# Kernel tuning notes

Hardware: AMD Instinct MI355X
Metric: run time of the kernel (lower is better)

The kernel has to match this reference:

```python
import jax, jax.numpy as jnp
import numpy as np
from jax import lax

T_STEPS = 16
TAU = 2.0
ALPHA = 4.0  # sigmoid surrogate sharpness
BN_EPS = 1e-5


def conv1d(x, w, b, stride, pad):
    # x: [N,C,L], w: [O,I,K]
    y = lax.conv_general_dilated(x, w, (stride,), [(pad, pad)],
                                 dimension_numbers=('NCH', 'OIH', 'NCH'))
    return y + b[None, :, None]


def maxpool1d(x):  # kernel 3, stride 2, pad 1 (pad value -inf via init)
    return lax.reduce_window(x, -jnp.inf, lax.max, (1, 1, 3), (1, 1, 2),
                             [(0, 0), (0, 0), (1, 1)])


def spike(x):  # heaviside forward (surrogate only matters for bwd)
    return (x >= 0).astype(x.dtype)


def lif(x_seq):
    # multi-step LIF: v += (x - v)/tau (v_reset=0), spike at v>=1, hard reset, detach_reset
    def step(v, x):
        v = v + (x - v) / TAU
        s = spike(v - 1.0)
        v = v * (1.0 - lax.stop_gradient(s))
        return v, s
    _, s_seq = lax.scan(step, jnp.zeros_like(x_seq[0]), x_seq)
    return s_seq


def seq_apply(f, xs):
    # apply stateless layer over [T,B,...] by folding T into batch
    T, B = xs.shape[0], xs.shape[1]
    y = f(xs.reshape((T * B,) + xs.shape[2:]))
    return y.reshape((T, B) + y.shape[1:])


def setup_inputs() -> dict:
    key = jax.random.key(0)
    ks = jax.random.split(key, 12)
    B, L = 256, 4097
    inp = {
        'x': jax.random.normal(ks[0], (B, L), jnp.float32),
        'conv0_w': jax.random.normal(ks[1], (16, 1, 7), jnp.float32) * 0.2,
        'conv0_b': jax.random.normal(ks[2], (16,), jnp.float32) * 0.1,
        'bn_g': jnp.ones((16,), jnp.float32),
        'bn_b': jnp.zeros((16,), jnp.float32),
        'bn_m': jax.random.normal(ks[3], (16,), jnp.float32) * 0.1,
        'bn_v': jnp.ones((16,), jnp.float32),
        'conv1_w': jax.random.normal(ks[4], (32, 16, 5), jnp.float32) * 0.1,
        'conv1_b': jax.random.normal(ks[5], (32,), jnp.float32) * 0.1,
        'conv2_w': jax.random.normal(ks[6], (64, 32, 3), jnp.float32) * 0.1,
        'conv2_b': jax.random.normal(ks[7], (64,), jnp.float32) * 0.1,
        'fc1_w': jax.random.normal(ks[8], (32, 64), jnp.float32) * 0.12,
        'fc1_b': jax.random.normal(ks[9], (32,), jnp.float32) * 0.1,
        'fc2_w': jax.random.normal(ks[10], (5, 32), jnp.float32) * 0.17,
        'fc2_b': jax.random.normal(ks[11], (5,), jnp.float32) * 0.1,
    }
    return inp


def reference(x, conv0_w, conv0_b, bn_g, bn_b, bn_m, bn_v,
              conv1_w, conv1_b, conv2_w, conv2_b,
              fc1_w, fc1_b, fc2_w, fc2_b):
    # ---- static encoder ----
    h = x[:, None, :]                                  # [B,1,4097]
    h = conv1d(h, conv0_w, conv0_b, 2, 3)              # [B,16,2049]
    h = (h - bn_m[None, :, None]) * lax.rsqrt(bn_v + BN_EPS)[None, :, None] \
        * bn_g[None, :, None] + bn_b[None, :, None]
    h = jax.nn.relu(h)
    h = maxpool1d(h)                                   # [B,16,1025]
    # ---- repeat over T timesteps ----
    hs = jnp.broadcast_to(h[None], (T_STEPS,) + h.shape)  # [T,B,16,1025]
    # ---- spiking trunk ----
    hs = seq_apply(lambda a: conv1d(a, conv1_w, conv1_b, 2, 2), hs)  # [T,B,32,513]
    hs = lif(hs)
    hs = seq_apply(maxpool1d, hs)                      # [T,B,32,257]
    hs = seq_apply(lambda a: conv1d(a, conv2_w, conv2_b, 2, 1), hs)  # [T,B,64,129]
    hs = lif(hs)
    # dropout: identity (inference); adaptive avg pool to 1 + flatten
    hs = hs.mean(axis=-1)                              # [T,B,64]
    # ---- classifier ----
    hs = jnp.einsum('tbd,od->tbo', hs, fc1_w) + fc1_b  # [T,B,32]
    hs = lif(hs)
    hs = jnp.einsum('tbd,od->tbo', hs, fc2_w) + fc2_b  # [T,B,5]
    return hs.mean(axis=0)                             # [B,5]
```

## Files before the change

### kernel.cpp

```cpp
#include <hip/hip_runtime.h>
#include <math.h>


#define NB 256
#define LX 4097
#define LQ 2049
#define LP 1025
#define LJ1 513
#define LP1 257
#define LJ2 129

#define M1S 520
#define S2R 132
#define HSW 260

typedef float f32x4 __attribute__((ext_vector_type(4)));

__global__ __launch_bounds__(256) void kF_front(const float* __restrict__ x,
                                                const float* __restrict__ w0,
                                                const float* __restrict__ b0,
                                                const float* __restrict__ bng,
                                                const float* __restrict__ bnb,
                                                const float* __restrict__ bnm,
                                                const float* __restrict__ bnv,
                                                const float* __restrict__ w1,
                                                const float* __restrict__ b1,
                                                unsigned short* __restrict__ m1,
                                                const float* __restrict__ w2,
                                                float* __restrict__ w2t) {
  __shared__ __align__(16) float xs[1052];
  __shared__ __align__(16) float hs[16 * HSW];
  __shared__ __align__(16) float wl[2560];
  __shared__ float w0s[112];
  __shared__ float cpar[64];
  __shared__ float rs_l[16];
  int bid = blockIdx.x;
  int b = bid / 5, jt = bid % 5;
  int J0 = jt * 128;
  int Pstart = 2 * J0 - 2;
  int tid = threadIdx.x;

  if (tid < 16) rs_l[tid] = (float)(1.0 / sqrt((double)bnv[tid] + 1e-5));
  {
    const float* xb = x + (size_t)b * LX;
    int xoff = 4 * Pstart - 5;
    for (int i = tid; i < 1052; i += 256) {
      int gi = xoff + i;
      xs[i] = (gi >= 0 && gi < LX) ? xb[gi] : 0.f;
    }
    for (int i = tid; i < 2560; i += 256) {
      int c = i & 31, r = i >> 5;
      wl[i] = w1[c * 80 + r];
    }
    if (tid < 112) w0s[tid] = w0[tid];
    if (tid >= 128 && tid < 192) {
      int i = tid - 128;
      int c = i >> 2, e = i & 3;
      float v = (e == 0) ? bnm[c] : (e == 1) ? bng[c] : (e == 2) ? bnb[c] : b0[c];
      cpar[i] = v;
    }
  }
  __syncthreads();

  for (int item = tid; item < 16 * 261; item += 256) {
    int c = item / 261, dp = item - c * 261;
    int p = Pstart + dp;
    float hm = 0.f;
    if (p >= 0 && p < LP) {
      const f32x4* xv = (const f32x4*)(xs + 4 * dp);
      f32x4 a = xv[0], bq = xv[1], cq = xv[2];
      float win[12] = {a.x, a.y, a.z, a.w, bq.x, bq.y, bq.z, bq.w,
                       cq.x, cq.y, cq.z, cq.w};
      float m = cpar[4 * c], g = cpar[4 * c + 1], bb = cpar[4 * c + 2],
            bc = cpar[4 * c + 3];
      float rs = rs_l[c];
      float wv[7];
#pragma unroll
      for (int k = 0; k < 7; ++k) wv[k] = w0s[c * 7 + k];
      float best = -INFINITY;
#pragma unroll
      for (int dq = -1; dq <= 1; ++dq) {
        int q = 2 * p + dq;
        if (q < 0 || q >= LQ) continue;
        float s = 0.f;
        int base = 2 * dq + 2;
#pragma unroll
        for (int k = 0; k < 7; ++k) s = fmaf(win[base + k], wv[k], s);
        float y = s + bc;
        y = (y - m) * rs * g + bb;
        y = fmaxf(y, 0.f);
        best = fmaxf(best, y);
      }
      hm = best;
    }
    hs[c * HSW + dp] = hm;
  }
  __syncthreads();

  {
    int c = tid & 31, jg = tid >> 5;
    int jbase = J0 + jg * 16;
    if (jbase <= 512) {
      float acc[16];
#pragma unroll
      for (int i = 0; i < 16; ++i) acc[i] = 0.f;

      for (int ic = 0; ic < 16; ++ic) {
        float win[36];
        const f32x4* row = (const f32x4*)(hs + ic * HSW + 32 * jg);
#pragma unroll
        for (int i = 0; i < 9; ++i) {
          f32x4 v = row[i];
          win[4 * i] = v.x; win[4 * i + 1] = v.y;
          win[4 * i + 2] = v.z; win[4 * i + 3] = v.w;
        }
        float wv[5];
#pragma unroll
        for (int k = 0; k < 5; ++k) wv[k] = wl[(ic * 5 + k) * 32 + c];
#pragma unroll
        for (int j = 0; j < 16; ++j) {
#pragma unroll
          for (int k = 0; k < 5; ++k) acc[j] = fmaf(win[2 * j + k], wv[k], acc[j]);
        }
      }

      float bc = b1[c];
      unsigned mskv[16];
#pragma unroll
      for (int j = 0; j < 16; ++j) {
        float xin = acc[j] + bc;
        float v = 0.f; unsigned mm = 0;
#pragma unroll
        for (int t = 0; t < 16; ++t) {
          v = v + (xin - v) * 0.5f;
          if (v >= 1.f) { mm |= (1u << t); v = 0.f; }
        }
        mskv[j] = mm;
      }
      size_t rowo = ((size_t)b * 32 + c) * M1S + jbase;
      if (jbase + 15 < LJ1) {
        uint4 u0, u1;
        u0.x = mskv[0] | (mskv[1] << 16);
        u0.y = mskv[2] | (mskv[3] << 16);
        u0.z = mskv[4] | (mskv[5] << 16);
        u0.w = mskv[6] | (mskv[7] << 16);
        u1.x = mskv[8] | (mskv[9] << 16);
        u1.y = mskv[10] | (mskv[11] << 16);
        u1.z = mskv[12] | (mskv[13] << 16);
        u1.w = mskv[14] | (mskv[15] << 16);
        *(uint4*)(m1 + rowo) = u0;
        *(uint4*)(m1 + rowo + 8) = u1;
      } else {
        for (int j = 0; j < 16; ++j)
          if (jbase + j < LJ1) m1[rowo + j] = (unsigned short)mskv[j];
      }
    }
  }

  if (bid < 16) {
    for (int idx = bid * 256 + tid; idx < 64 * 32 * 3; idx += 4096) {
      int k = idx % 3; int r = idx / 3; int c = r % 32; int oc = r / 32;
      w2t[(c * 3 + k) * 64 + oc] = w2[idx];
    }
  }
}

__global__ __launch_bounds__(256) void kD_conv2_lif(const unsigned short* __restrict__ m1,
                                                    const float* __restrict__ w2t_g,
                                                    const float* __restrict__ b2,
                                                    unsigned short* __restrict__ s2) {
  __shared__ __align__(16) float F[288 * 20];
  __shared__ unsigned mval[288];
  __shared__ unsigned short mbuf[32 * 20];
  int bid = blockIdx.x;
  int b = bid / 33, jt = bid % 33;
  int j0 = jt * 4;
  int tid = threadIdx.x;
  int w = tid >> 6;
  int lane = tid & 63;

  const unsigned short* m1b = m1 + (size_t)b * 32 * M1S;
  int qbase = 4 * j0 - 3;
  for (int i = tid; i < 1024; i += 256) {
    int c = i >> 5, u = i & 31;
    if (u < 20) {
      int q = qbase + u;
      mbuf[c * 20 + u] = (q >= 0 && q <= 512) ? m1b[(size_t)c * M1S + q] : (unsigned short)0;
    }
  }
  __syncthreads();

  for (int it = tid; it < 288; it += 256) {
    int c = it / 9, idx = it - c * 9;
    int p = 2 * j0 - 1 + idx;
    unsigned m = 0;
    if (p >= 0 && p < LP1) {
      const unsigned short* mr = mbuf + c * 20;
      int l0 = 2 * idx;
      m = (unsigned)mr[l0] | (unsigned)mr[l0 + 1] | (unsigned)mr[l0 + 2];
    }
    mval[it] = m;
    f32x4* Fr = (f32x4*)(F + it * 20);
    f32x4 f0, f1, f2, f3;
    f0.x = (float)(m & 1u);         f0.y = (float)((m >> 1) & 1u);
    f0.z = (float)((m >> 2) & 1u);  f0.w = (float)((m >> 3) & 1u);
    f1.x = (float)((m >> 4) & 1u);  f1.y = (float)((m >> 5) & 1u);
    f1.z = (float)((m >> 6) & 1u);  f1.w = (float)((m >> 7) & 1u);
    f2.x = (float)((m >> 8) & 1u);  f2.y = (float)((m >> 9) & 1u);
    f2.z = (float)((m >> 10) & 1u); f2.w = (float)((m >> 11) & 1u);
    f3.x = (float)((m >> 12) & 1u); f3.y = (float)((m >> 13) & 1u);
    f3.z = (float)((m >> 14) & 1u); f3.w = (float)((m >> 15) & 1u);
    Fr[0] = f0; Fr[1] = f1; Fr[2] = f2; Fr[3] = f3;
  }
  __syncthreads();

  unsigned bits;
  {
    bool nz = false;
    if (lane < 32) {
      int base9 = lane * 9 + 2 * w;
      nz = (mval[base9] | mval[base9 + 1] | mval[base9 + 2]) != 0u;
    }
    bits = (unsigned)__ballot(nz);
  }

  float acc[16];
#pragma unroll
  for (int t = 0; t < 16; ++t) acc[t] = 0.f;

  const float* wrow = w2t_g + lane;
  while (bits) {
    int c = __builtin_ctz(bits);
    bits &= bits - 1;
    int base9 = c * 9 + 2 * w;
    unsigned mv0 = mval[base9];
    unsigned mv1 = mval[base9 + 1];
    unsigned mv2 = mval[base9 + 2];
    const float* wr = wrow + c * 192;
    const float* Fb = F + base9 * 20;
    if (mv0) {
      float wv = wr[0];
      const f32x4* Fp = (const f32x4*)Fb;
      f32x4 fv[4];
      fv[0] = Fp[0]; fv[1] = Fp[1]; fv[2] = Fp[2]; fv[3] = Fp[3];
#pragma unroll
      for (int t = 0; t < 16; ++t) acc[t] = fmaf(wv, fv[t >> 2][t & 3], acc[t]);
    }
    if (mv1) {
      float wv = wr[64];
      const f32x4* Fp = (const f32x4*)(Fb + 20);
      f32x4 fv[4];
      fv[0] = Fp[0]; fv[1] = Fp[1]; fv[2] = Fp[2]; fv[3] = Fp[3];
#pragma unroll
      for (int t = 0; t < 16; ++t) acc[t] = fmaf(wv, fv[t >> 2][t & 3], acc[t]);
    }
    if (mv2) {
      float wv = wr[128];
      const f32x4* Fp = (const f32x4*)(Fb + 40);
      f32x4 fv[4];
      fv[0] = Fp[0]; fv[1] = Fp[1]; fv[2] = Fp[2]; fv[3] = Fp[3];
#pragma unroll
      for (int t = 0; t < 16; ++t) acc[t] = fmaf(wv, fv[t >> 2][t & 3], acc[t]);
    }
  }

  int j = j0 + w;
  if (j < LJ2) {
    float bc = b2[lane];
    float v = 0.f; unsigned mm = 0;
#pragma unroll
    for (int t = 0; t < 16; ++t) {
      float xin = acc[t] + bc;
      v = v + (xin - v) * 0.5f;
      if (v >= 1.f) { mm |= (1u << t); v = 0.f; }
    }
    s2[((size_t)b * S2R + j) * 64 + lane] = (unsigned short)mm;
  }
}

__global__ __launch_bounds__(256) void kE_head(const unsigned short* __restrict__ s2,
                                               const float* __restrict__ fc1w,
                                               const float* __restrict__ fc1b,
                                               const float* __restrict__ fc2w,
                                               const float* __restrict__ fc2b,
                                               float* __restrict__ out) {
  __shared__ float meanL[16][64];
  __shared__ unsigned s3m[32];
  int b = blockIdx.x;
  int tid = threadIdx.x;
  int oc = tid >> 2, part = tid & 3;

  int jstart = (part == 0) ? 0 : 33 + (part - 1) * 32;
  int jcount = (part == 0) ? 33 : 32;
  const unsigned short* base = s2 + (size_t)b * S2R * 64 + oc;
  int cnt[16];
#pragma unroll
  for (int t = 0; t < 16; ++t) cnt[t] = 0;
  for (int u = 0; u < jcount; ++u) {
    unsigned m = base[(size_t)(jstart + u) * 64];
#pragma unroll
    for (int t = 0; t < 16; ++t) cnt[t] += (int)((m >> t) & 1u);
  }
#pragma unroll
  for (int t = 0; t < 16; ++t) {
    cnt[t] += __shfl_xor(cnt[t], 1);
    cnt[t] += __shfl_xor(cnt[t], 2);
  }
  if (part == 0) {
#pragma unroll
    for (int t = 0; t < 16; ++t) meanL[t][oc] = (float)cnt[t] / 129.f;
  }
  __syncthreads();

  if (tid < 32) {
    int o = tid;
    const float* wrow = fc1w + o * 64;
    float bb = fc1b[o];
    float v = 0.f;
    unsigned msk = 0;
    for (int t = 0; t < 16; ++t) {
      float s = 0.f;
      for (int d = 0; d < 64; ++d) s = fmaf(meanL[t][d], wrow[d], s);
      float xin = s + bb;
      v = v + (xin - v) * 0.5f;
      if (v >= 1.f) { msk |= (1u << t); v = 0.f; }
    }
    s3m[o] = msk;
  }
  __syncthreads();

  if (tid < 5) {
    int q = tid;
    const float* wrow = fc2w + q * 32;
    float bb = fc2b[q];
    float accs = 0.f;
    for (int t = 0; t < 16; ++t) {
      float s = 0.f;
      for (int o = 0; o < 32; ++o) s += (((s3m[o] >> t) & 1u) ? wrow[o] : 0.f);
      accs += (s + bb);
    }
    out[b * 5 + q] = accs / 16.f;
  }
}

extern "C" void kernel_launch(void* const* d_in, const int* in_sizes, int n_in,
                              void* d_out, int out_size, void* d_ws, size_t ws_size,
                              hipStream_t stream) {
  const float* x   = (const float*)d_in[0];
  const float* w0  = (const float*)d_in[1];
  const float* b0  = (const float*)d_in[2];
  const float* bng = (const float*)d_in[3];
  const float* bnb = (const float*)d_in[4];
  const float* bnm = (const float*)d_in[5];
  const float* bnv = (const float*)d_in[6];
  const float* w1  = (const float*)d_in[7];
  const float* b1  = (const float*)d_in[8];
  const float* w2  = (const float*)d_in[9];
  const float* b2  = (const float*)d_in[10];
  const float* f1w = (const float*)d_in[11];
  const float* f1b = (const float*)d_in[12];
  const float* f2w = (const float*)d_in[13];
  const float* f2b = (const float*)d_in[14];
  float* out = (float*)d_out;

  char* ws = (char*)d_ws;
  size_t sz_m1 = (size_t)NB * 32 * M1S * 2;
  size_t sz_s2 = (size_t)NB * S2R * 64 * 2;
  size_t off_s2 = sz_m1;
  size_t off_w2 = off_s2 + sz_s2;
  if (ws_size < off_w2 + 6144 * 4) return;

  unsigned short* m1 = (unsigned short*)ws;
  unsigned short* s2 = (unsigned short*)(ws + off_s2);
  float* w2t = (float*)(ws + off_w2);

  kF_front<<<NB * 5, 256, 0, stream>>>(x, w0, b0, bng, bnb, bnm, bnv, w1, b1, m1, w2, w2t);
  kD_conv2_lif<<<NB * 33, 256, 0, stream>>>(m1, w2t, b2, s2);
  kE_head<<<NB, 256, 0, stream>>>(s2, f1w, f1b, f2w, f2b, out);
}
```

Baseline: 121.1 us.

## Halve conv2 block size with 2 outputs per thread; restructure front and head reductions

The conv2+LIF kernel now runs 128 threads per block. Each lane computes two output channels for one output position, so each F row loaded from LDS feeds two accumulator sets, and the per-channel zero-skip becomes a coarser whole-row check. The front encoder loop assigns one channel per 16-thread group and hoists per-channel weights and BN parameters out of the item loop. The head now does a coalesced per-warp count with an LDS reduction instead of shuffles. The costs are higher register pressure and fewer skipped FMAs in kD.

```diff
diff --git a/kernel.cpp b/kernel.cpp
--- a/kernel.cpp
+++ b/kernel.cpp
@@ -62,38 +62,43 @@
   }
   __syncthreads();
 
-  for (int item = tid; item < 16 * 261; item += 256) {
-    int c = item / 261, dp = item - c * 261;
-    int p = Pstart + dp;
-    float hm = 0.f;
-    if (p >= 0 && p < LP) {
-      const f32x4* xv = (const f32x4*)(xs + 4 * dp);
-      f32x4 a = xv[0], bq = xv[1], cq = xv[2];
-      float win[12] = {a.x, a.y, a.z, a.w, bq.x, bq.y, bq.z, bq.w,
-                       cq.x, cq.y, cq.z, cq.w};
-      float m = cpar[4 * c], g = cpar[4 * c + 1], bb = cpar[4 * c + 2],
-            bc = cpar[4 * c + 3];
-      float rs = rs_l[c];
-      float wv[7];
-#pragma unroll
-      for (int k = 0; k < 7; ++k) wv[k] = w0s[c * 7 + k];
-      float best = -INFINITY;
-#pragma unroll
-      for (int dq = -1; dq <= 1; ++dq) {
-        int q = 2 * p + dq;
-        if (q < 0 || q >= LQ) continue;
-        float s = 0.f;
-        int base = 2 * dq + 2;
-#pragma unroll
-        for (int k = 0; k < 7; ++k) s = fmaf(win[base + k], wv[k], s);
-        float y = s + bc;
-        y = (y - m) * rs * g + bb;
-        y = fmaxf(y, 0.f);
-        best = fmaxf(best, y);
-      }
-      hm = best;
-    }
-    hs[c * HSW + dp] = hm;
+  {
+    int c2 = tid >> 4, g2 = tid & 15;
+    float m = cpar[4 * c2], g = cpar[4 * c2 + 1], bb = cpar[4 * c2 + 2],
+          bc = cpar[4 * c2 + 3];
+    float rs = rs_l[c2];
+    float wv[7];
+#pragma unroll
+    for (int k = 0; k < 7; ++k) wv[k] = w0s[c2 * 7 + k];
+#pragma unroll
+    for (int i = 0; i < 17; ++i) {
+      int dp = g2 * 17 + i;
+      if (dp >= 261) break;
+      int p = Pstart + dp;
+      float hm = 0.f;
+      if (p >= 0 && p < LP) {
+        const f32x4* xv = (const f32x4*)(xs + 4 * dp);
+        f32x4 a = xv[0], bq = xv[1], cq = xv[2];
+        float win[12] = {a.x, a.y, a.z, a.w, bq.x, bq.y, bq.z, bq.w,
+                         cq.x, cq.y, cq.z, cq.w};
+        float best = -INFINITY;
+#pragma unroll
+        for (int dq = -1; dq <= 1; ++dq) {
+          int q = 2 * p + dq;
+          if (q < 0 || q >= LQ) continue;
+          float s = 0.f;
+          int base = 2 * dq + 2;
+#pragma unroll
+          for (int k = 0; k < 7; ++k) s = fmaf(win[base + k], wv[k], s);
+          float y = s + bc;
+          y = (y - m) * rs * g + bb;
+          y = fmaxf(y, 0.f);
+          best = fmaxf(best, y);
+        }
+        hm = best;
+      }
+      hs[c2 * HSW + dp] = hm;
+    }
   }
   __syncthreads();
 
@@ -165,7 +170,7 @@
   }
 }
 
-__global__ __launch_bounds__(256) void kD_conv2_lif(const unsigned short* __restrict__ m1,
+__global__ __launch_bounds__(128) void kD_conv2_lif(const unsigned short* __restrict__ m1,
                                                     const float* __restrict__ w2t_g,
                                                     const float* __restrict__ b2,
                                                     unsigned short* __restrict__ s2) {
@@ -174,25 +179,27 @@
   __shared__ unsigned short mbuf[32 * 20];
   int bid = blockIdx.x;
   int b = bid / 33, jt = bid % 33;
-  int j0 = jt * 4;
+  int J0 = jt * 4;
   int tid = threadIdx.x;
   int w = tid >> 6;
   int lane = tid & 63;
+  int wh = lane >> 5;
+  int oc0 = lane & 31;
 
   const unsigned short* m1b = m1 + (size_t)b * 32 * M1S;
-  int qbase = 4 * j0 - 3;
-  for (int i = tid; i < 1024; i += 256) {
-    int c = i >> 5, u = i & 31;
-    if (u < 20) {
+  int qbase = 4 * J0 - 3;
+  for (int i = tid; i < 640; i += 128) {
+    int c = i / 20, u = i - c * 20;
+    if (u < 19) {
       int q = qbase + u;
       mbuf[c * 20 + u] = (q >= 0 && q <= 512) ? m1b[(size_t)c * M1S + q] : (unsigned short)0;
     }
   }
   __syncthreads();
 
-  for (int it = tid; it < 288; it += 256) {
+  for (int it = tid; it < 288; it += 128) {
     int c = it / 9, idx = it - c * 9;
-    int p = 2 * j0 - 1 + idx;
+    int p = 2 * J0 - 1 + idx;
     unsigned m = 0;
     if (p >= 0 && p < LP1) {
       const unsigned short* mr = mbuf + c * 20;
@@ -218,63 +225,79 @@
   {
     bool nz = false;
     if (lane < 32) {
-      int base9 = lane * 9 + 2 * w;
-      nz = (mval[base9] | mval[base9 + 1] | mval[base9 + 2]) != 0u;
+      int mb = lane * 9 + 4 * w;
+      unsigned o = mval[mb] | mval[mb + 1] | mval[mb + 2] | mval[mb + 3] | mval[mb + 4];
+      nz = (o != 0u);
     }
     bits = (unsigned)__ballot(nz);
   }
 
-  float acc[16];
-#pragma unroll
-  for (int t = 0; t < 16; ++t) acc[t] = 0.f;
-
-  const float* wrow = w2t_g + lane;
+  float acc0[16], acc1[16];
+#pragma unroll
+  for (int t = 0; t < 16; ++t) { acc0[t] = 0.f; acc1[t] = 0.f; }
+
+  int lp0 = 4 * w + 2 * wh;
+  const float* Fbase = F + lp0 * 20;
+  const float* wbase = w2t_g + oc0;
+
   while (bits) {
     int c = __builtin_ctz(bits);
     bits &= bits - 1;
-    int base9 = c * 9 + 2 * w;
-    unsigned mv0 = mval[base9];
-    unsigned mv1 = mval[base9 + 1];
-    unsigned mv2 = mval[base9 + 2];
-    const float* wr = wrow + c * 192;
-    const float* Fb = F + base9 * 20;
-    if (mv0) {
-      float wv = wr[0];
-      const f32x4* Fp = (const f32x4*)Fb;
-      f32x4 fv[4];
-      fv[0] = Fp[0]; fv[1] = Fp[1]; fv[2] = Fp[2]; fv[3] = Fp[3];
-#pragma unroll
-      for (int t = 0; t < 16; ++t) acc[t] = fmaf(wv, fv[t >> 2][t & 3], acc[t]);
-    }
-    if (mv1) {
-      float wv = wr[64];
-      const f32x4* Fp = (const f32x4*)(Fb + 20);
-      f32x4 fv[4];
-      fv[0] = Fp[0]; fv[1] = Fp[1]; fv[2] = Fp[2]; fv[3] = Fp[3];
-#pragma unroll
-      for (int t = 0; t < 16; ++t) acc[t] = fmaf(wv, fv[t >> 2][t & 3], acc[t]);
-    }
-    if (mv2) {
-      float wv = wr[128];
-      const f32x4* Fp = (const f32x4*)(Fb + 40);
-      f32x4 fv[4];
-      fv[0] = Fp[0]; fv[1] = Fp[1]; fv[2] = Fp[2]; fv[3] = Fp[3];
-#pragma unroll
-      for (int t = 0; t < 16; ++t) acc[t] = fmaf(wv, fv[t >> 2][t & 3], acc[t]);
-    }
-  }
-
-  int j = j0 + w;
+    const float* wr = wbase + c * 192;
+    float wa0 = wr[0],  wb0 = wr[64], wc0 = wr[128];
+    float wa1 = wr[32], wb1 = wr[96], wc1 = wr[160];
+    const f32x4* Fp = (const f32x4*)(Fbase + c * 180);
+    f32x4 ra0 = Fp[0],  ra1 = Fp[1],  ra2 = Fp[2],  ra3 = Fp[3];
+    f32x4 rb0 = Fp[5],  rb1 = Fp[6],  rb2 = Fp[7],  rb3 = Fp[8];
+    f32x4 rc0 = Fp[10], rc1 = Fp[11], rc2 = Fp[12], rc3 = Fp[13];
+    float fa[16] = {ra0.x, ra0.y, ra0.z, ra0.w, ra1.x, ra1.y, ra1.z, ra1.w,
+                    ra2.x, ra2.y, ra2.z, ra2.w, ra3.x, ra3.y, ra3.z, ra3.w};
+    float fb[16] = {rb0.x, rb0.y, rb0.z, rb0.w, rb1.x, rb1.y, rb1.z, rb1.w,
+                    rb2.x, rb2.y, rb2.z, rb2.w, rb3.x, rb3.y, rb3.z, rb3.w};
+    float fc[16] = {rc0.x, rc0.y, rc0.z, rc0.w, rc1.x, rc1.y, rc1.z, rc1.w,
+                    rc2.x, rc2.y, rc2.z, rc2.w, rc3.x, rc3.y, rc3.z, rc3.w};
+#pragma unroll
+    for (int t = 0; t < 16; ++t) {
+      acc0[t] = fmaf(wa0, fa[t], acc0[t]);
+      acc1[t] = fmaf(wa1, fa[t], acc1[t]);
+    }
+#pragma unroll
+    for (int t = 0; t < 16; ++t) {
+      acc0[t] = fmaf(wb0, fb[t], acc0[t]);
+      acc1[t] = fmaf(wb1, fb[t], acc1[t]);
+    }
+#pragma unroll
+    for (int t = 0; t < 16; ++t) {
+      acc0[t] = fmaf(wc0, fc[t], acc0[t]);
+      acc1[t] = fmaf(wc1, fc[t], acc1[t]);
+    }
+  }
+
+  int j = J0 + 2 * w + wh;
   if (j < LJ2) {
-    float bc = b2[lane];
-    float v = 0.f; unsigned mm = 0;
-#pragma unroll
-    for (int t = 0; t < 16; ++t) {
-      float xin = acc[t] + bc;
-      v = v + (xin - v) * 0.5f;
-      if (v >= 1.f) { mm |= (1u << t); v = 0.f; }
-    }
-    s2[((size_t)b * S2R + j) * 64 + lane] = (unsigned short)mm;
+    unsigned short* srow = s2 + ((size_t)b * S2R + j) * 64;
+    {
+      float bc = b2[oc0];
+      float v = 0.f; unsigned mm = 0;
+#pragma unroll
+      for (int t = 0; t < 16; ++t) {
+        float xin = acc0[t] + bc;
+        v = v + (xin - v) * 0.5f;
+        if (v >= 1.f) { mm |= (1u << t); v = 0.f; }
+      }
+      srow[oc0] = (unsigned short)mm;
+    }
+    {
+      float bc = b2[oc0 + 32];
+      float v = 0.f; unsigned mm = 0;
+#pragma unroll
+      for (int t = 0; t < 16; ++t) {
+        float xin = acc1[t] + bc;
+        v = v + (xin - v) * 0.5f;
+        if (v >= 1.f) { mm |= (1u << t); v = 0.f; }
+      }
+      srow[oc0 + 32] = (unsigned short)mm;
+    }
   }
 }
 
@@ -284,31 +307,34 @@
                                                const float* __restrict__ fc2w,
                                                const float* __restrict__ fc2b,
                                                float* __restrict__ out) {
+  __shared__ unsigned cntL[4][16][64];
   __shared__ float meanL[16][64];
   __shared__ unsigned s3m[32];
   int b = blockIdx.x;
   int tid = threadIdx.x;
-  int oc = tid >> 2, part = tid & 3;
-
-  int jstart = (part == 0) ? 0 : 33 + (part - 1) * 32;
-  int jcount = (part == 0) ? 33 : 32;
-  const unsigned short* base = s2 + (size_t)b * S2R * 64 + oc;
-  int cnt[16];
+  int w = tid >> 6, lane = tid & 63;
+
+  int j0 = (w == 0) ? 0 : 33 + 32 * (w - 1);
+  int jc = (w == 0) ? 33 : 32;
+  const unsigned short* base = s2 + (size_t)b * S2R * 64 + lane;
+  unsigned cnt[16];
 #pragma unroll
   for (int t = 0; t < 16; ++t) cnt[t] = 0;
-  for (int u = 0; u < jcount; ++u) {
-    unsigned m = base[(size_t)(jstart + u) * 64];
-#pragma unroll
-    for (int t = 0; t < 16; ++t) cnt[t] += (int)((m >> t) & 1u);
-  }
-#pragma unroll
-  for (int t = 0; t < 16; ++t) {
-    cnt[t] += __shfl_xor(cnt[t], 1);
-    cnt[t] += __shfl_xor(cnt[t], 2);
-  }
-  if (part == 0) {
-#pragma unroll
-    for (int t = 0; t < 16; ++t) meanL[t][oc] = (float)cnt[t] / 129.f;
+  for (int u = 0; u < jc; ++u) {
+    unsigned m = base[(size_t)(j0 + u) * 64];
+#pragma unroll
+    for (int t = 0; t < 16; ++t) cnt[t] += (m >> t) & 1u;
+  }
+#pragma unroll
+  for (int t = 0; t < 16; ++t) cntL[w][t][lane] = cnt[t];
+  __syncthreads();
+
+#pragma unroll
+  for (int i = 0; i < 4; ++i) {
+    int idx = tid + 256 * i;
+    int t = idx >> 6, oc = idx & 63;
+    unsigned s = cntL[0][t][oc] + cntL[1][t][oc] + cntL[2][t][oc] + cntL[3][t][oc];
+    meanL[t][oc] = (float)s / 129.f;
   }
   __syncthreads();
 
@@ -375,6 +401,6 @@
   float* w2t = (float*)(ws + off_w2);
 
   kF_front<<<NB * 5, 256, 0, stream>>>(x, w0, b0, bng, bnb, bnm, bnv, w1, b1, m1, w2, w2t);
-  kD_conv2_lif<<<NB * 33, 256, 0, stream>>>(m1, w2t, b2, s2);
+  kD_conv2_lif<<<NB * 33, 128, 0, stream>>>(m1, w2t, b2, s2);
   kE_head<<<NB, 256, 0, stream>>>(s2, f1w, f1b, f2w, f2b, out);
 }
```

After: 121.0 us. Within noise of the previous version (-0.0%).
